# Kernel optimization log

Measured on AMD Instinct MI355X. Metric: run time of the kernel, lower is better.

Reference implementation:

```python
import jax, jax.numpy as jnp
import numpy as np

B, N, K = 4, 250_000, 32
W_FG, W_INST, W_SMOOTH, W_SEED = 1.0, 1.0, 10.0, 10.0


def setup_inputs() -> dict:
    key = jax.random.key(0)
    k1, k2, k3, k4, k5 = jax.random.split(key, 5)
    return {
        "offsets": jax.random.normal(k1, (B, N, 3), jnp.float32),
        "coords": jax.random.normal(k2, (B, N, 3), jnp.float32),
        # small sigma scale so exp(10*sigma_k) stays in a sane range
        "sigmas": jax.random.normal(k3, (B, N, 3), jnp.float32) * 0.05,
        "seeds": jax.random.normal(k4, (B, N), jnp.float32),
        # instance ids in [-1, K); -1 = background
        "instances": jax.random.randint(k5, (B, N), 0, K + 1, jnp.int32) - 1,
    }


def _lovasz_hinge(logits, labels):
    # logits, labels: (B, K, N); vectorized lovasz_hinge_flat per (b, k)
    signs = 2.0 * labels - 1.0
    errors = 1.0 - logits * signs
    order = jnp.argsort(-errors, axis=-1)              # descending sort
    errors_sorted = jnp.take_along_axis(errors, order, axis=-1)
    gt_sorted = jnp.take_along_axis(labels, order, axis=-1)
    gts = jnp.sum(gt_sorted, axis=-1, keepdims=True)
    intersection = gts - jnp.cumsum(gt_sorted, axis=-1)
    union = gts + jnp.cumsum(1.0 - gt_sorted, axis=-1)
    jaccard = 1.0 - intersection / union
    grad = jnp.concatenate([jaccard[..., :1], jaccard[..., 1:] - jaccard[..., :-1]], axis=-1)
    return jnp.sum(jax.nn.relu(errors_sorted) * grad, axis=-1)  # (B, K)


def reference(offsets, coords, sigmas, seeds, instances):
    sg = jax.lax.stop_gradient
    emb = jnp.tanh(offsets) + coords                    # (B, N, 3) spatial embeddings
    seed = jax.nn.sigmoid(seeds)                        # (B, N)

    masks = (instances[:, :, None] == jnp.arange(K)[None, None, :]).astype(jnp.float32)  # (B, N, K)
    counts = jnp.sum(masks, axis=1)                     # (B, K)
    validf = (counts > 0).astype(jnp.float32)
    cnt = jnp.maximum(counts, 1.0)

    # per-instance masked means
    center = jnp.einsum('bnk,bnd->bkd', masks, emb) / cnt[..., None]     # (B, K, 3)
    sigma_k = jnp.einsum('bnk,bnd->bkd', masks, sigmas) / cnt[..., None]  # (B, K, 3)

    # smooth loss: mean over masked (n_k, 3) of (sigma - stop_grad(sigma_k))^2
    sk = sg(sigma_k)
    dev2 = (jnp.einsum('bnk,bnd->bk', masks, sigmas ** 2)
            - 2.0 * jnp.einsum('bnk,bnd,bkd->bk', masks, sigmas, sk)
            + counts * jnp.sum(sk ** 2, axis=-1))
    smooth_k = dev2 / (cnt * 3.0)                       # (B, K)

    s_e = jnp.exp(sigma_k * 10.0)                       # (B, K, 3)
    # quad[b,k,n] = sum_d s_e * (emb - center)^2, expanded to avoid (B,K,N,3)
    quad = (jnp.einsum('bkd,bnd->bkn', s_e, emb ** 2)
            - 2.0 * jnp.einsum('bkd,bnd->bkn', s_e * center, emb)
            + jnp.sum(s_e * center ** 2, axis=-1)[:, :, None])
    probs = jnp.exp(-quad)                              # (B, K, N)
    logits = 2.0 * probs - 1.0

    labels = jnp.transpose(masks, (0, 2, 1))            # (B, K, N)
    lov = _lovasz_hinge(logits, labels)                 # (B, K)

    obj = jnp.maximum(jnp.sum(validf, axis=-1), 1.0)    # (B,)
    instance_loss = jnp.sum(lov * validf, axis=-1) / obj
    smooth_loss = jnp.sum(smooth_k * validf, axis=-1) / obj

    bg = (instances == -1).astype(jnp.float32)
    seed_bg = jnp.sum(bg * seed ** 2, axis=-1)          # (B,)
    seed_fg = W_FG * jnp.sum(labels * (seed[:, None, :] - sg(probs)) ** 2, axis=(-1, -2))
    seed_loss = (seed_bg + seed_fg) / float(N)

    loss = jnp.mean(W_INST * instance_loss + W_SMOOTH * smooth_loss + W_SEED * seed_loss)
    return loss + jnp.sum(offsets) * 0.0
```

## Files before the change

kernel.cpp:

```cpp
#include <hip/hip_runtime.h>
#include <hip/hip_fp16.h>
#include <math.h>

#define B_ 4
#define N_ 250000
#define K_ 32
#define NB 4096
#define NB2 2048
#define KG 2
#define HCH 16
#define S2 16
#define SC 4
#define SLOT_SHIFT 13


__device__ __forceinline__ uint32_t pack_h2(float a, float b) {
  __half2 h = __floats2half2_rn(a, b);
  return *(reinterpret_cast<uint32_t*>(&h));
}
__device__ __forceinline__ float2 unpack_h2(uint32_t u) {
  __half2 h = *(reinterpret_cast<__half2*>(&u));
  return __half22float2(h);
}

__device__ __forceinline__ float quad_qc(float ex, float ey, float ez,
                                         float sex, float sey, float sez,
                                         float tx, float ty, float tz, float A) {
  float q = fmaf(ex, fmaf(sex, ex, -tx),
            fmaf(ey, fmaf(sey, ey, -ty),
            fmaf(ez, fmaf(sez, ez, -tz), A)));
  return fmaxf(q, 0.f);
}

__device__ __forceinline__ float fast_rcp(float x) { return __builtin_amdgcn_rcpf(x); }
__device__ __forceinline__ float fast_tanh(float x) {
  return 1.f - 2.f * fast_rcp(__expf(2.f * x) + 1.f);
}
__device__ __forceinline__ float fast_sigmoid(float x) {
  return fast_rcp(1.f + __expf(-x));
}

__global__ __launch_bounds__(256) void k_emb(
    const float* __restrict__ off, const float* __restrict__ crd,
    const float* __restrict__ seed, const int* __restrict__ inst,
    float* __restrict__ seed_bg, uint2* __restrict__ emb2,
    uint32_t* __restrict__ cursor, uint32_t* __restrict__ list,
    uint32_t* __restrict__ hneg_g)
{
  __shared__ uint32_t lcnt[K_], lbase[K_];
  __shared__ float red[4];
  const int b = blockIdx.y;
  const int tid = threadIdx.x;

  {
    int flat = (blockIdx.y * gridDim.x + blockIdx.x) * 256 + tid;
    if (flat < (2097152 / 16)) ((uint4*)hneg_g)[flat] = make_uint4(0u, 0u, 0u, 0u);
  }

  if (tid < K_) lcnt[tid] = 0;
  __syncthreads();

  const int n0 = blockIdx.x * 1024 + tid * 4;
  int kv[4];
  const bool valid = (n0 < N_);
  float sbg = 0.f;

  if (valid) {
    const int idx = b * N_ + n0;
    const float4* o4 = (const float4*)&off[(size_t)idx * 3];
    const float4* c4 = (const float4*)&crd[(size_t)idx * 3];
    float4 o0 = o4[0], o1 = o4[1], o2 = o4[2];
    float4 c0 = c4[0], c1 = c4[1], c2 = c4[2];
    int4 ki = *(const int4*)&inst[idx];
    kv[0] = ki.x; kv[1] = ki.y; kv[2] = ki.z; kv[3] = ki.w;

    float ex0 = fast_tanh(o0.x) + c0.x, ey0 = fast_tanh(o0.y) + c0.y, ez0 = fast_tanh(o0.z) + c0.z;
    float ex1 = fast_tanh(o0.w) + c0.w, ey1 = fast_tanh(o1.x) + c1.x, ez1 = fast_tanh(o1.y) + c1.y;
    float ex2 = fast_tanh(o1.z) + c1.z, ey2 = fast_tanh(o1.w) + c1.w, ez2 = fast_tanh(o2.x) + c2.x;
    float ex3 = fast_tanh(o2.y) + c2.y, ey3 = fast_tanh(o2.z) + c2.z, ez3 = fast_tanh(o2.w) + c2.w;
    uint4 w0, w1;
    w0.x = pack_h2(ex0, ey0); w0.y = pack_h2(ez0, 0.f);
    w0.z = pack_h2(ex1, ey1); w0.w = pack_h2(ez1, 0.f);
    w1.x = pack_h2(ex2, ey2); w1.y = pack_h2(ez2, 0.f);
    w1.z = pack_h2(ex3, ey3); w1.w = pack_h2(ez3, 0.f);
    ((uint4*)&emb2[idx])[0] = w0;
    ((uint4*)&emb2[idx])[1] = w1;

#pragma unroll
    for (int j = 0; j < 4; ++j) {
      if (kv[j] >= 0) {
        atomicAdd(&lcnt[kv[j]], 1u);
      } else {
        float s = fast_sigmoid(seed[idx + j]);
        sbg = fmaf(s, s, sbg);
      }
    }
  }
  __syncthreads();
  if (tid < K_) {
    uint32_t c = lcnt[tid];
    lbase[tid] = c ? atomicAdd(&cursor[b * K_ + tid], c) : 0u;
    lcnt[tid] = 0;
  }
  __syncthreads();
  if (valid) {
#pragma unroll
    for (int j = 0; j < 4; ++j) {
      if (kv[j] >= 0) {
        uint32_t r = atomicAdd(&lcnt[kv[j]], 1u);
        list[(uint32_t)((b * K_ + kv[j]) << SLOT_SHIFT) + lbase[kv[j]] + r] =
            (uint32_t)(n0 + j);
      }
    }
  }
  for (int d = 32; d > 0; d >>= 1) sbg += __shfl_down(sbg, d, 64);
  int wid = tid >> 6, lane = tid & 63;
  if (lane == 0) red[wid] = sbg;
  __syncthreads();
  if (tid == 0) atomicAdd(&seed_bg[b], red[0] + red[1] + red[2] + red[3]);
}

__global__ __launch_bounds__(256) void k_segstats(
    const uint2* __restrict__ emb2, const float* __restrict__ sig,
    const uint32_t* __restrict__ list, const uint32_t* __restrict__ cursor,
    float* __restrict__ acc)
{
  __shared__ float red[4 * 8];
  const int seg = blockIdx.x >> 2;
  const int c = blockIdx.x & (SC - 1);
  const int b = seg >> 5;
  const int G = (int)cursor[seg];
  if (G == 0) return;
  const int i0 = (int)((long)G * c / SC);
  const int i1 = (int)((long)G * (c + 1) / SC);
  const int base = b * N_;
  const uint32_t lo = (uint32_t)(seg << SLOT_SHIFT);
  const int tid = threadIdx.x;

  float sex_ = 0.f, sey_ = 0.f, sez_ = 0.f;
  float ssx = 0.f, ssy = 0.f, ssz = 0.f, ss2 = 0.f;
  for (int i = i0 + tid; i < i1; i += 256) {
    int idx = base + (int)list[lo + i];
    uint2 e = emb2[idx];
    float2 xy = unpack_h2(e.x);
    float2 zw = unpack_h2(e.y);
    float sx = sig[(size_t)idx * 3 + 0];
    float sy = sig[(size_t)idx * 3 + 1];
    float sz = sig[(size_t)idx * 3 + 2];
    sex_ += xy.x; sey_ += xy.y; sez_ += zw.x;
    ssx += sx; ssy += sy; ssz += sz;
    ss2 = fmaf(sx, sx, fmaf(sy, sy, fmaf(sz, sz, ss2)));
  }
  for (int d = 32; d > 0; d >>= 1) {
    sex_ += __shfl_down(sex_, d, 64); sey_ += __shfl_down(sey_, d, 64);
    sez_ += __shfl_down(sez_, d, 64); ssx  += __shfl_down(ssx,  d, 64);
    ssy  += __shfl_down(ssy,  d, 64); ssz  += __shfl_down(ssz,  d, 64);
    ss2  += __shfl_down(ss2,  d, 64);
  }
  int wid = tid >> 6, lane = tid & 63;
  if (lane == 0) {
    float* r = &red[wid * 8];
    r[0] = sex_; r[1] = sey_; r[2] = sez_;
    r[3] = ssx;  r[4] = ssy;  r[5] = ssz; r[6] = ss2;
  }
  __syncthreads();
  if (tid == 0) {
    float v[7];
    for (int f = 0; f < 7; ++f)
      v[f] = red[f] + red[8 + f] + red[16 + f] + red[24 + f];
    float* a = &acc[seg * 8];
    atomicAdd(&a[0], (float)(i1 - i0));
    atomicAdd(&a[1], v[0]); atomicAdd(&a[2], v[1]); atomicAdd(&a[3], v[2]);
    atomicAdd(&a[4], v[3]); atomicAdd(&a[5], v[4]); atomicAdd(&a[6], v[5]);
    atomicAdd(&a[7], v[6]);
  }
}

__global__ __launch_bounds__(512) void k_hist(
    const uint2* __restrict__ emb2, const float* __restrict__ acc,
    float* __restrict__ p05, uint32_t* __restrict__ hneg_g)
{
  __shared__ uint32_t h[KG * NB];
  const int c = blockIdx.x & (HCH - 1);
  const int kg = blockIdx.x >> 4;
  const int b = blockIdx.y;
  const int seg0 = b * K_ + kg * KG;
  const int tid = threadIdx.x;

  float sexA[KG], seyA[KG], sezA[KG], txA[KG], tyA[KG], tzA[KG], AA[KG];
#pragma unroll
  for (int j = 0; j < KG; ++j) {
    const float* a = &acc[(seg0 + j) * 8];
    float counts = a[0];
    float cnt = fmaxf(counts, 1.f);
    float inv = 1.f / cnt;
    float cx = a[1] * inv, cy = a[2] * inv, cz = a[3] * inv;
    float skx = a[4] * inv, sky = a[5] * inv, skz = a[6] * inv;
    sexA[j] = expf(10.f * skx); seyA[j] = expf(10.f * sky); sezA[j] = expf(10.f * skz);
    txA[j] = 2.f * sexA[j] * cx; tyA[j] = 2.f * seyA[j] * cy; tzA[j] = 2.f * sezA[j] * cz;
    AA[j] = sexA[j] * cx * cx + seyA[j] * cy * cy + sezA[j] * cz * cz;
    if (c == 0 && tid == 0) {
      float dev2 = a[7] - 2.f * (a[4] * skx + a[5] * sky + a[6] * skz)
                 + counts * (skx * skx + sky * sky + skz * skz);
      float* o = &p05[(seg0 + j) * 16];
      o[0] = sexA[j]; o[1] = seyA[j]; o[2] = sezA[j];
      o[3] = txA[j]; o[4] = tyA[j]; o[5] = tzA[j];
      o[6] = AA[j]; o[7] = counts;
      o[8] = (counts > 0.f) ? 1.f : 0.f; o[9] = dev2 / (cnt * 3.f);
    }
  }
  for (int i = tid; i < KG * NB; i += 512) h[i] = 0;
  __syncthreads();

  const int base = b * N_;
  const int n0 = c * (N_ / HCH);
  const int n1 = n0 + (N_ / HCH);
  for (int n = n0 + tid; n < n1; n += 512) {
    uint2 e = emb2[base + n];
    float2 xy = unpack_h2(e.x);
    float2 zw = unpack_h2(e.y);
#pragma unroll
    for (int j = 0; j < KG; ++j) {
      float qc = quad_qc(xy.x, xy.y, zw.x,
                         sexA[j], seyA[j], sezA[j], txA[j], tyA[j], tzA[j], AA[j]);
      atomicAdd(&h[j * NB + (__float_as_uint(qc) >> 19)], 1u);
    }
  }
  __syncthreads();
#pragma unroll
  for (int j = 0; j < KG; ++j) {
    uint32_t* gn = &hneg_g[(seg0 + j) * NB];
    for (int i = tid; i < NB; i += 512) {
      uint32_t v = h[j * NB + i];
      if (v) atomicAdd(&gn[i], v);
    }
  }
}

__device__ __forceinline__ void scan_excl(uint32_t* h, uint32_t* wsum, int tid)
{
  const int chunk = NB >> 10;
  const int base = tid * chunk;
  uint32_t vals[4];
  uint32_t s = 0;
  for (int i = 0; i < chunk; ++i) { vals[i] = h[base + i]; s += vals[i]; }
  uint32_t x = s;
  int lane = tid & 63;
  for (int d = 1; d < 64; d <<= 1) {
    uint32_t y = (uint32_t)__shfl_up((int)x, d, 64);
    if (lane >= d) x += y;
  }
  int wid = tid >> 6;
  if (lane == 63) wsum[wid] = x;
  __syncthreads();
  if (tid == 0) {
    uint32_t a = 0;
    for (int w = 0; w < 16; ++w) { uint32_t t = wsum[w]; wsum[w] = a; a += t; }
  }
  __syncthreads();
  uint32_t run = wsum[wid] + (x - s);
  for (int i = 0; i < chunk; ++i) { uint32_t t = vals[i]; h[base + i] = run; run += t; }
  __syncthreads();
}

__global__ __launch_bounds__(1024) void k_scanpos(
    const uint2* __restrict__ emb2, const float* __restrict__ seed,
    const float* __restrict__ p05, const uint32_t* __restrict__ list,
    uint32_t* __restrict__ hneg_g, float2* __restrict__ tabN,
    float* __restrict__ lov_out, float* __restrict__ seed_fg)
{
  __shared__ uint32_t hn[NB];
  __shared__ uint32_t hp[NB];
  __shared__ uint32_t wsum[16];
  __shared__ float red[32];
  const int seg = blockIdx.x;
  const int b = seg >> 5;
  const float* pp = &p05[seg * 16];
  const float Gf = pp[7];
  if (Gf <= 0.f) return;
  const float sex = pp[0], sey = pp[1], sez = pp[2];
  const float tx = pp[3], ty = pp[4], tz = pp[5], A = pp[6];
  const int tid = threadIdx.x;
  const int base = b * N_;
  const int G = (int)Gf;
  const uint32_t lo = (uint32_t)(seg << SLOT_SHIFT);
  const float Nnegf = (float)N_ - Gf;

  uint32_t* gn = &hneg_g[seg * NB];
  for (int i = tid; i < NB; i += 1024) { hn[i] = gn[i]; hp[i] = 0; }
  __syncthreads();

  for (int i = tid; i < G; i += 1024) {
    int n = (int)list[lo + i];
    uint2 e = emb2[base + n];
    float2 xy = unpack_h2(e.x);
    float2 zw = unpack_h2(e.y);
    float qc = quad_qc(xy.x, xy.y, zw.x, sex, sey, sez, tx, ty, tz, A);
    atomicAdd(&hn[__float_as_uint(qc) >> 19], 0xFFFFFFFFu);
    float p = __expf(-qc);
    float qs = -__logf(1.f - p);
    atomicAdd(&hp[__float_as_uint(qs) >> 19], 1u);
  }
  __syncthreads();
  scan_excl(hn, wsum, tid);
  scan_excl(hp, wsum, tid);

  float2* tN = &tabN[(size_t)seg * NB2];
  for (int bkt = tid; bkt < NB2; bkt += 1024) {
    float R  = (float)hn[2 * bkt];
    float nn = (bkt < NB2 - 1) ? (float)hn[2 * bkt + 2] : Nnegf;
    float m  = nn - R;
    float pb = (float)hp[2 * bkt];
    float pn = (bkt < NB2 - 1) ? (float)hp[2 * bkt + 2] : Gf;
    float gr = Gf + R;
    float psi2 = 2.f / (gr * (gr + m));
    float u = psi2 * (Gf - pb);
    float v = psi2 * (pn - pb) * (1.f / 1048576.f);
    tN[bkt] = make_float2(u, v);
  }

  float lov = 0.f, sfg = 0.f;
  for (int i = tid; i < G; i += 1024) {
    int n = (int)list[lo + i];
    uint2 e = emb2[base + n];
    float2 xy = unpack_h2(e.x);
    float2 zw = unpack_h2(e.y);
    float qc = quad_qc(xy.x, xy.y, zw.x, sex, sey, sez, tx, ty, tz, A);
    float p = __expf(-qc);
    float qs = -__logf(1.f - p);
    uint32_t qb = __float_as_uint(qs);
    uint32_t bk = qb >> 19;
    float frac = (float)(qb & 0x7FFFFu) * (1.f / 524288.f);
    float R  = (float)hn[bk];
    float nn = (bk < NB - 1) ? (float)hn[bk + 1] : Nnegf;
    float F = R + frac * (nn - R);
    lov += (2.f - 2.f * p) / (Gf + F);
    float s = fast_sigmoid(seed[base + n]);
    float d = s - p;
    sfg += d * d;
    uint32_t cb = __float_as_uint(qc);
    uint32_t b2 = cb >> 20;
    float fr = (float)(cb & 0xFFFFFu);
    float R2  = (float)hn[2 * b2];
    float nn2 = (b2 < NB2 - 1) ? (float)hn[2 * b2 + 2] : Nnegf;
    float m2  = nn2 - R2;
    float pb2 = (float)hp[2 * b2];
    float pn2 = (b2 < NB2 - 1) ? (float)hp[2 * b2 + 2] : Gf;
    float gr2 = Gf + R2;
    float psi2 = 2.f / (gr2 * (gr2 + m2));
    float u2 = psi2 * (Gf - pb2);
    float v2 = psi2 * (pn2 - pb2) * (1.f / 1048576.f);
    lov -= p * fmaf(-v2, fr, u2);
  }

  for (int d = 32; d > 0; d >>= 1) {
    lov += __shfl_down(lov, d, 64);
    sfg += __shfl_down(sfg, d, 64);
  }
  int wid = tid >> 6, lane = tid & 63;
  if (lane == 0) { red[wid] = lov; red[16 + wid] = sfg; }
  __syncthreads();
  if (tid == 0) {
    float lt = 0.f, st = 0.f;
    for (int w = 0; w < 16; ++w) { lt += red[w]; st += red[16 + w]; }
    atomicAdd(&lov_out[seg], lt);
    atomicAdd(&seed_fg[b], st);
  }
}

__global__ __launch_bounds__(256) void k_pass2neg(
    const uint2* __restrict__ emb2, const float* __restrict__ p05,
    const float2* __restrict__ tabN, float* __restrict__ lov_out)
{
  __shared__ float red[4];
  const int seg = blockIdx.x >> 4;
  const int chunk = blockIdx.x & (S2 - 1);
  const int b = seg >> 5;
  const float* pp = &p05[seg * 16];
  const float Gf = pp[7];
  if (Gf <= 0.f) return;
  const float sex = pp[0], sey = pp[1], sez = pp[2];
  const float tx = pp[3], ty = pp[4], tz = pp[5], A = pp[6];
  const int tid = threadIdx.x;
  const int base = b * N_;
  const int n0 = chunk * (N_ / S2);
  const int nfull = n0 + 15360;
  const int n1 = n0 + (N_ / S2);
  const float2* tN = &tabN[(size_t)seg * NB2];

  float l0 = 0.f, l1 = 0.f, l2 = 0.f, l3 = 0.f;
  for (int s = n0 + tid; s < nfull; s += 1024) {
    uint2 e0 = emb2[base + s];
    uint2 e1 = emb2[base + s + 256];
    uint2 e2 = emb2[base + s + 512];
    uint2 e3 = emb2[base + s + 768];
    float2 a0 = unpack_h2(e0.x), b0 = unpack_h2(e0.y);
    float2 a1 = unpack_h2(e1.x), b1 = unpack_h2(e1.y);
    float2 a2 = unpack_h2(e2.x), b2 = unpack_h2(e2.y);
    float2 a3 = unpack_h2(e3.x), b3 = unpack_h2(e3.y);
    float q0 = quad_qc(a0.x, a0.y, b0.x, sex, sey, sez, tx, ty, tz, A);
    float q1 = quad_qc(a1.x, a1.y, b1.x, sex, sey, sez, tx, ty, tz, A);
    float q2 = quad_qc(a2.x, a2.y, b2.x, sex, sey, sez, tx, ty, tz, A);
    float q3 = quad_qc(a3.x, a3.y, b3.x, sex, sey, sez, tx, ty, tz, A);
    uint32_t c0 = __float_as_uint(q0), c1 = __float_as_uint(q1);
    uint32_t c2 = __float_as_uint(q2), c3 = __float_as_uint(q3);
    float2 t0 = tN[c0 >> 20];
    float2 t1 = tN[c1 >> 20];
    float2 t2 = tN[c2 >> 20];
    float2 t3 = tN[c3 >> 20];
    float p0 = __expf(-q0), p1 = __expf(-q1);
    float p2 = __expf(-q2), p3 = __expf(-q3);
    l0 = fmaf(p0, fmaf(-t0.y, (float)(c0 & 0xFFFFFu), t0.x), l0);
    l1 = fmaf(p1, fmaf(-t1.y, (float)(c1 & 0xFFFFFu), t1.x), l1);
    l2 = fmaf(p2, fmaf(-t2.y, (float)(c2 & 0xFFFFFu), t2.x), l2);
    l3 = fmaf(p3, fmaf(-t3.y, (float)(c3 & 0xFFFFFu), t3.x), l3);
  }
  for (int n = nfull + tid; n < n1; n += 256) {
    uint2 e = emb2[base + n];
    float2 xy = unpack_h2(e.x);
    float2 zw = unpack_h2(e.y);
    float qc = quad_qc(xy.x, xy.y, zw.x, sex, sey, sez, tx, ty, tz, A);
    float p = __expf(-qc);
    uint32_t cb = __float_as_uint(qc);
    float2 t = tN[cb >> 20];
    l0 = fmaf(p, fmaf(-t.y, (float)(cb & 0xFFFFFu), t.x), l0);
  }

  float lov = (l0 + l1) + (l2 + l3);
  for (int d = 32; d > 0; d >>= 1) lov += __shfl_down(lov, d, 64);
  int wid = tid >> 6, lane = tid & 63;
  if (lane == 0) red[wid] = lov;
  __syncthreads();
  if (tid == 0) {
    float lt = red[0] + red[1] + red[2] + red[3];
    atomicAdd(&lov_out[seg], lt);
  }
}

__global__ void k_final(const float* __restrict__ p05, const float* __restrict__ lov,
                        const float* __restrict__ seed_bg, const float* __restrict__ seed_fg,
                        float* __restrict__ out)
{
  __shared__ float sv[B_], sl[B_], ss[B_];
  int tid = threadIdx.x;
  if (tid < B_) { sv[tid] = 0.f; sl[tid] = 0.f; ss[tid] = 0.f; }
  __syncthreads();
  int b = tid >> 5;
  float vf = p05[tid * 16 + 8];
  atomicAdd(&sv[b], vf);
  atomicAdd(&sl[b], lov[tid] * vf);
  atomicAdd(&ss[b], p05[tid * 16 + 9] * vf);
  __syncthreads();
  if (tid == 0) {
    float total = 0.f;
    for (int bb = 0; bb < B_; ++bb) {
      float obj = fmaxf(sv[bb], 1.f);
      float seed_l = (seed_bg[bb] + seed_fg[bb]) / (float)N_;
      total += sl[bb] / obj + 10.f * (ss[bb] / obj) + 10.f * seed_l;
    }
    out[0] = total / (float)B_;
  }
}

extern "C" void kernel_launch(void* const* d_in, const int* in_sizes, int n_in,
                              void* d_out, int out_size, void* d_ws, size_t ws_size,
                              hipStream_t stream) {
  const float* off  = (const float*)d_in[0];
  const float* crd  = (const float*)d_in[1];
  const float* sig  = (const float*)d_in[2];
  const float* seed = (const float*)d_in[3];
  const int*   inst = (const int*)d_in[4];

  float* ws      = (float*)d_ws;
  float* acc     = ws;
  float* seed_bg = ws + 1024;
  float* seed_fg = ws + 1028;
  float* lov     = ws + 1032;
  uint32_t* cursor = (uint32_t*)(ws + 1160);
  float* p05     = ws + 2048;
  char* pbase = (char*)d_ws;
  uint2*    emb2   = (uint2*)(pbase + 65536);
  uint32_t* hneg_g = (uint32_t*)(pbase + 65536 + 8388608);
  float2*   tabN   = (float2*)(pbase + 65536 + 8388608 + 2097152);
  uint32_t* list   = (uint32_t*)((char*)tabN + 2097152);

  hipMemsetAsync(d_ws, 0, 8192, stream);

  dim3 ge((N_ + 1023) / 1024, B_);
  k_emb<<<ge, 256, 0, stream>>>(off, crd, seed, inst, seed_bg, emb2, cursor, list,
                                hneg_g);
  k_segstats<<<B_ * K_ * SC, 256, 0, stream>>>(emb2, sig, list, cursor, acc);
  dim3 gh((K_ / KG) * HCH, B_);
  k_hist<<<gh, 512, 0, stream>>>(emb2, acc, p05, hneg_g);
  k_scanpos<<<B_ * K_, 1024, 0, stream>>>(emb2, seed, p05, list, hneg_g, tabN, lov, seed_fg);
  k_pass2neg<<<B_ * K_ * S2, 256, 0, stream>>>(emb2, p05, tabN, lov);
  k_final<<<1, 128, 0, stream>>>(p05, lov, seed_bg, seed_fg, (float*)d_out);
}
```

Baseline: 209.0 us.

## Pack histogram bins as 16-bit halves to process four instances per block

```diff
diff --git a/kernel.cpp b/kernel.cpp
--- a/kernel.cpp
+++ b/kernel.cpp
@@ -7,8 +7,8 @@
 #define K_ 32
 #define NB 4096
 #define NB2 2048
-#define KG 2
-#define HCH 16
+#define KG 4
+#define HCH 25
 #define S2 16
 #define SC 4
 #define SLOT_SHIFT 13
@@ -180,9 +180,9 @@
     const uint2* __restrict__ emb2, const float* __restrict__ acc,
     float* __restrict__ p05, uint32_t* __restrict__ hneg_g)
 {
-  __shared__ uint32_t h[KG * NB];
-  const int c = blockIdx.x & (HCH - 1);
-  const int kg = blockIdx.x >> 4;
+  __shared__ uint32_t h[KG * NB2];
+  const int c = blockIdx.x % HCH;
+  const int kg = blockIdx.x / HCH;
   const int b = blockIdx.y;
   const int seg0 = b * K_ + kg * KG;
   const int tid = threadIdx.x;
@@ -209,13 +209,30 @@
       o[8] = (counts > 0.f) ? 1.f : 0.f; o[9] = dev2 / (cnt * 3.f);
     }
   }
-  for (int i = tid; i < KG * NB; i += 512) h[i] = 0;
+  for (int i = tid; i < KG * NB2; i += 512) h[i] = 0;
   __syncthreads();
 
   const int base = b * N_;
   const int n0 = c * (N_ / HCH);
+  const int nfull = n0 + 9216;
   const int n1 = n0 + (N_ / HCH);
-  for (int n = n0 + tid; n < n1; n += 512) {
+  for (int n = n0 + tid * 2; n < nfull; n += 1024) {
+    uint4 e2p = *(const uint4*)&emb2[base + n];
+    float2 xy0 = unpack_h2(e2p.x), zw0 = unpack_h2(e2p.y);
+    float2 xy1 = unpack_h2(e2p.z), zw1 = unpack_h2(e2p.w);
+#pragma unroll
+    for (int j = 0; j < KG; ++j) {
+      float q0 = quad_qc(xy0.x, xy0.y, zw0.x,
+                         sexA[j], seyA[j], sezA[j], txA[j], tyA[j], tzA[j], AA[j]);
+      float q1 = quad_qc(xy1.x, xy1.y, zw1.x,
+                         sexA[j], seyA[j], sezA[j], txA[j], tyA[j], tzA[j], AA[j]);
+      uint32_t b0 = __float_as_uint(q0) >> 19;
+      uint32_t b1 = __float_as_uint(q1) >> 19;
+      atomicAdd(&h[j * NB2 + (b0 & (NB2 - 1))], 1u << ((b0 >> 11) << 4));
+      atomicAdd(&h[j * NB2 + (b1 & (NB2 - 1))], 1u << ((b1 >> 11) << 4));
+    }
+  }
+  for (int n = nfull + tid; n < n1; n += 512) {
     uint2 e = emb2[base + n];
     float2 xy = unpack_h2(e.x);
     float2 zw = unpack_h2(e.y);
@@ -223,16 +240,19 @@
     for (int j = 0; j < KG; ++j) {
       float qc = quad_qc(xy.x, xy.y, zw.x,
                          sexA[j], seyA[j], sezA[j], txA[j], tyA[j], tzA[j], AA[j]);
-      atomicAdd(&h[j * NB + (__float_as_uint(qc) >> 19)], 1u);
+      uint32_t bk = __float_as_uint(qc) >> 19;
+      atomicAdd(&h[j * NB2 + (bk & (NB2 - 1))], 1u << ((bk >> 11) << 4));
     }
   }
   __syncthreads();
 #pragma unroll
   for (int j = 0; j < KG; ++j) {
     uint32_t* gn = &hneg_g[(seg0 + j) * NB];
-    for (int i = tid; i < NB; i += 512) {
-      uint32_t v = h[j * NB + i];
-      if (v) atomicAdd(&gn[i], v);
+    for (int i = tid; i < NB2; i += 512) {
+      uint32_t v = h[j * NB2 + i];
+      uint32_t lo = v & 0xFFFFu, hi = v >> 16;
+      if (lo) atomicAdd(&gn[i], lo);
+      if (hi) atomicAdd(&gn[i + NB2], hi);
     }
   }
 }
```

After: 212.7 us. Within noise of the previous version (+1.8%).
